# Kernel tuning notes

Measured on AMD Instinct MI355X. Metric: run time of the kernel, lower is better.

Reference implementation:

```python
import jax, jax.numpy as jnp
import numpy as np


def setup_inputs() -> dict:
    key = jax.random.key(0)
    ks = jax.random.split(key, 6)
    B, L, R, A, D = 256, 196, 1024, 512, 2048
    return {
        "h": jax.random.normal(ks[0], (B, R), dtype=jnp.float32),
        "att_feats1": jax.random.normal(ks[1], (B, L, D), dtype=jnp.float32),
        "att_feats2": jax.random.normal(ks[2], (B, L, A), dtype=jnp.float32),
        "att_masks": jnp.ones((B, L), dtype=jnp.float32),
        "W_h": jax.random.normal(ks[3], (R, A), dtype=jnp.float32) * (1.0 / np.sqrt(R)),
        "b_h": jnp.zeros((A,), dtype=jnp.float32),
        "w_a": jax.random.normal(ks[4], (A,), dtype=jnp.float32) * (1.0 / np.sqrt(A)),
        "b_a": jnp.zeros((), dtype=jnp.float32),
    }


def reference(h, att_feats1, att_feats2, att_masks, W_h, b_h, w_a, b_a):
    # att_h = h2att(h): [B, A]
    att_h = h @ W_h + b_h
    # dot = alpha_net(tanh(att_feats2 + att_h[:, None, :])): [B, L]
    dot = jnp.einsum("bla,a->bl", jnp.tanh(att_feats2 + att_h[:, None, :]), w_a) + b_a
    weight = jax.nn.softmax(dot, axis=1)  # [B, L]
    # masked renormalization
    weight = weight * att_masks
    weight = weight / jnp.sum(weight, axis=1, keepdims=True)
    # weighted sum over regions: [B, D]
    att = jnp.einsum("bl,bld->bd", weight, att_feats1)
    return att
```

## Files before the change

kernel.cpp:

```cpp
#include <hip/hip_runtime.h>

#define BB 256
#define LL 196
#define RR 1024
#define AA 512
#define DD 2048

__device__ __forceinline__ float fast_tanh(float x) {
    float e = __expf(2.0f * x);
    return 1.0f - 2.0f * __builtin_amdgcn_rcpf(e + 1.0f);
}

__global__ __launch_bounds__(256) void gemm_hWh(const float* __restrict__ h,
                                                const float* __restrict__ W,
                                                const float* __restrict__ bh,
                                                float* __restrict__ out) {
    __shared__ float As[32][33];
    __shared__ float Bs[32][33];
    const int bn = blockIdx.x;
    const int bm = blockIdx.y;
    const int t  = threadIdx.x;
    const int ty = t >> 4, tx = t & 15;
    const int lr = t >> 3;
    const int lc = (t & 7) * 4;

    float acc00 = 0.f, acc01 = 0.f, acc10 = 0.f, acc11 = 0.f;

    for (int k0 = 0; k0 < RR; k0 += 32) {
        float4 a4 = *(const float4*)&h[(size_t)(bm * 32 + lr) * RR + k0 + lc];
        float4 b4 = *(const float4*)&W[(size_t)(k0 + lr) * AA + bn * 32 + lc];
        As[lr][lc + 0] = a4.x; As[lr][lc + 1] = a4.y;
        As[lr][lc + 2] = a4.z; As[lr][lc + 3] = a4.w;
        Bs[lr][lc + 0] = b4.x; Bs[lr][lc + 1] = b4.y;
        Bs[lr][lc + 2] = b4.z; Bs[lr][lc + 3] = b4.w;
        __syncthreads();
#pragma unroll
        for (int kk = 0; kk < 32; ++kk) {
            float a0 = As[ty * 2 + 0][kk];
            float a1 = As[ty * 2 + 1][kk];
            float b0 = Bs[kk][tx * 2 + 0];
            float b1 = Bs[kk][tx * 2 + 1];
            acc00 += a0 * b0; acc01 += a0 * b1;
            acc10 += a1 * b0; acc11 += a1 * b1;
        }
        __syncthreads();
    }
    const int gm = bm * 32 + ty * 2;
    const int gn = bn * 32 + tx * 2;
    out[(size_t)(gm + 0) * AA + gn + 0] = acc00 + bh[gn + 0];
    out[(size_t)(gm + 0) * AA + gn + 1] = acc01 + bh[gn + 1];
    out[(size_t)(gm + 1) * AA + gn + 0] = acc10 + bh[gn + 0];
    out[(size_t)(gm + 1) * AA + gn + 1] = acc11 + bh[gn + 1];
}

__global__ __launch_bounds__(1024) void attn_fused(
    const float* __restrict__ f1,
    const float* __restrict__ f2,
    const float* __restrict__ masks,
    const float* __restrict__ att_h,
    const float* __restrict__ w_a,
    float* __restrict__ out)
{
    __shared__ float dot[LL];
    __shared__ float red[256];
    __shared__ float w[LL];
    __shared__ float sacc[512 * 4];

    const int b = blockIdx.x;
    const int t = threadIdx.x;
    const int wave = t >> 6, lane = t & 63;

    const float4* ah4 = (const float4*)(att_h + (size_t)b * AA);
    const float4* wa4 = (const float4*)w_a;
    const float4 a0 = ah4[lane * 2], a1 = ah4[lane * 2 + 1];
    const float4 w0 = wa4[lane * 2], w1 = wa4[lane * 2 + 1];

    const float4* f2b = (const float4*)(f2 + (size_t)b * LL * AA);

    for (int l = wave; l < LL; l += 16) {
        float4 v0 = f2b[l * 128 + lane * 2];
        float4 v1 = f2b[l * 128 + lane * 2 + 1];
        float p = fast_tanh(v0.x + a0.x) * w0.x
                + fast_tanh(v0.y + a0.y) * w0.y
                + fast_tanh(v0.z + a0.z) * w0.z
                + fast_tanh(v0.w + a0.w) * w0.w
                + fast_tanh(v1.x + a1.x) * w1.x
                + fast_tanh(v1.y + a1.y) * w1.y
                + fast_tanh(v1.z + a1.z) * w1.z
                + fast_tanh(v1.w + a1.w) * w1.w;
#pragma unroll
        for (int off = 32; off; off >>= 1) p += __shfl_down(p, off);
        if (lane == 0) dot[l] = p;
    }
    __syncthreads();

    if (t < 256) red[t] = (t < LL) ? dot[t] : -1e30f;
    __syncthreads();
#pragma unroll
    for (int s = 128; s; s >>= 1) {
        if (t < s) red[t] = fmaxf(red[t], red[t + s]);
        __syncthreads();
    }
    const float m = red[0];
    __syncthreads();
    float e = 0.f;
    if (t < LL) e = __expf(dot[t] - m) * masks[(size_t)b * LL + t];
    if (t < 256) red[t] = e;
    __syncthreads();
#pragma unroll
    for (int s = 128; s; s >>= 1) {
        if (t < s) red[t] += red[t + s];
        __syncthreads();
    }
    if (t < LL) w[t] = e * (1.0f / red[0]);
    __syncthreads();

    const int u    = t & 511;
    const int half = t >> 9;
    const float4* f1b = (const float4*)(f1 + (size_t)b * LL * DD) + u;
    float4 acc = {0.f, 0.f, 0.f, 0.f};
    const int l0 = half * 98;
#pragma unroll 7
    for (int i = 0; i < 98; ++i) {
        const int l = l0 + i;
        float4 v = f1b[(size_t)l * 512];
        const float wl = w[l];
        acc.x += wl * v.x; acc.y += wl * v.y;
        acc.z += wl * v.z; acc.w += wl * v.w;
    }
    if (half == 1) *(float4*)&sacc[u * 4] = acc;
    __syncthreads();
    if (half == 0) {
        float4 o = *(float4*)&sacc[u * 4];
        acc.x += o.x; acc.y += o.y; acc.z += o.z; acc.w += o.w;
        *(float4*)&out[(size_t)b * DD + u * 4] = acc;
    }
}

extern "C" void kernel_launch(void* const* d_in, const int* in_sizes, int n_in,
                              void* d_out, int out_size, void* d_ws, size_t ws_size,
                              hipStream_t stream) {
    const float* h   = (const float*)d_in[0];
    const float* f1  = (const float*)d_in[1];
    const float* f2  = (const float*)d_in[2];
    const float* msk = (const float*)d_in[3];
    const float* W   = (const float*)d_in[4];
    const float* bh  = (const float*)d_in[5];
    const float* wa  = (const float*)d_in[6];
    float* out = (float*)d_out;

    float* att_h = (float*)d_ws;

    gemm_hWh<<<dim3(16, 8), 256, 0, stream>>>(h, W, bh, att_h);
    attn_fused<<<BB, 1024, 0, stream>>>(f1, f2, msk, att_h, wa, out);
}
```

Before: 634.3 us.

## Fuse h@W_h projection into attention kernel, drop separate GEMM launch

Removes the separate tiled GEMM kernel and computes each batch row's att_h inside the attention block. Each block stages its h row in shared memory and performs a 1024x512 matvec against W_h, split across two thread halves, before the tanh/score phase. This removes a kernel launch and the att_h round trip through global memory. In exchange every block rereads all of W_h (2 MB, likely served from L2) and does the matvec serially ahead of the main streaming work.

```diff
diff --git a/kernel.cpp b/kernel.cpp
--- a/kernel.cpp
+++ b/kernel.cpp
@@ -11,56 +11,18 @@
     return 1.0f - 2.0f * __builtin_amdgcn_rcpf(e + 1.0f);
 }
 
-__global__ __launch_bounds__(256) void gemm_hWh(const float* __restrict__ h,
-                                                const float* __restrict__ W,
-                                                const float* __restrict__ bh,
-                                                float* __restrict__ out) {
-    __shared__ float As[32][33];
-    __shared__ float Bs[32][33];
-    const int bn = blockIdx.x;
-    const int bm = blockIdx.y;
-    const int t  = threadIdx.x;
-    const int ty = t >> 4, tx = t & 15;
-    const int lr = t >> 3;
-    const int lc = (t & 7) * 4;
-
-    float acc00 = 0.f, acc01 = 0.f, acc10 = 0.f, acc11 = 0.f;
-
-    for (int k0 = 0; k0 < RR; k0 += 32) {
-        float4 a4 = *(const float4*)&h[(size_t)(bm * 32 + lr) * RR + k0 + lc];
-        float4 b4 = *(const float4*)&W[(size_t)(k0 + lr) * AA + bn * 32 + lc];
-        As[lr][lc + 0] = a4.x; As[lr][lc + 1] = a4.y;
-        As[lr][lc + 2] = a4.z; As[lr][lc + 3] = a4.w;
-        Bs[lr][lc + 0] = b4.x; Bs[lr][lc + 1] = b4.y;
-        Bs[lr][lc + 2] = b4.z; Bs[lr][lc + 3] = b4.w;
-        __syncthreads();
-#pragma unroll
-        for (int kk = 0; kk < 32; ++kk) {
-            float a0 = As[ty * 2 + 0][kk];
-            float a1 = As[ty * 2 + 1][kk];
-            float b0 = Bs[kk][tx * 2 + 0];
-            float b1 = Bs[kk][tx * 2 + 1];
-            acc00 += a0 * b0; acc01 += a0 * b1;
-            acc10 += a1 * b0; acc11 += a1 * b1;
-        }
-        __syncthreads();
-    }
-    const int gm = bm * 32 + ty * 2;
-    const int gn = bn * 32 + tx * 2;
-    out[(size_t)(gm + 0) * AA + gn + 0] = acc00 + bh[gn + 0];
-    out[(size_t)(gm + 0) * AA + gn + 1] = acc01 + bh[gn + 1];
-    out[(size_t)(gm + 1) * AA + gn + 0] = acc10 + bh[gn + 0];
-    out[(size_t)(gm + 1) * AA + gn + 1] = acc11 + bh[gn + 1];
-}
-
 __global__ __launch_bounds__(1024) void attn_fused(
+    const float* __restrict__ h,
     const float* __restrict__ f1,
     const float* __restrict__ f2,
     const float* __restrict__ masks,
-    const float* __restrict__ att_h,
+    const float* __restrict__ W,
+    const float* __restrict__ bh,
     const float* __restrict__ w_a,
     float* __restrict__ out)
 {
+    __shared__ float hs[RR];
+    __shared__ float ah[AA];
     __shared__ float dot[LL];
     __shared__ float red[256];
     __shared__ float w[LL];
@@ -70,7 +32,30 @@
     const int t = threadIdx.x;
     const int wave = t >> 6, lane = t & 63;
 
-    const float4* ah4 = (const float4*)(att_h + (size_t)b * AA);
+    if (t < 256) ((float4*)hs)[t] = ((const float4*)(h + (size_t)b * RR))[t];
+    __syncthreads();
+
+    {
+        const int n  = t & 511;
+        const int kh = t >> 9;
+        const float4* hs4 = (const float4*)hs;
+        float acc = 0.f;
+#pragma unroll 2
+        for (int k4 = kh * 128; k4 < kh * 128 + 128; ++k4) {
+            const float4 hv = hs4[k4];
+            const float* Wk = W + (size_t)(k4 * 4) * AA + n;
+            acc += hv.x * Wk[0 * AA];
+            acc += hv.y * Wk[1 * AA];
+            acc += hv.z * Wk[2 * AA];
+            acc += hv.w * Wk[3 * AA];
+        }
+        if (kh == 1) sacc[n] = acc;
+        __syncthreads();
+        if (kh == 0) ah[n] = acc + sacc[n] + bh[n];
+    }
+    __syncthreads();
+
+    const float4* ah4 = (const float4*)ah;
     const float4* wa4 = (const float4*)w_a;
     const float4 a0 = ah4[lane * 2], a1 = ah4[lane * 2 + 1];
     const float4 w0 = wa4[lane * 2], w1 = wa4[lane * 2 + 1];
@@ -149,8 +134,5 @@
     const float* wa  = (const float*)d_in[6];
     float* out = (float*)d_out;
 
-    float* att_h = (float*)d_ws;
-
-    gemm_hWh<<<dim3(16, 8), 256, 0, stream>>>(h, W, bh, att_h);
-    attn_fused<<<BB, 1024, 0, stream>>>(f1, f2, msk, att_h, wa, out);
+    attn_fused<<<BB, 1024, 0, stream>>>(h, f1, f2, msk, W, bh, wa, out);
 }
```

Result: no change. 631.3 us (-0.5%).

## Replace two-phase softmax with tiled online softmax overlapping score and feature streams

Applied to the files above, without the earlier changes.

The attention kernel now processes regions in tiles of 16 with an online (running max/sum) softmax. Each tile's scores are computed while the previous tile's weighted f1 accumulation runs, using double-buffered shared memory. This removes the separate max/sum tree reductions and the serialized score-then-gather phases, so f2 and f1 loads can overlap. In exchange it adds per-tile rescaling, a barrier per tile, and exp recomputation by every thread.

```diff
diff --git a/kernel.cpp b/kernel.cpp
--- a/kernel.cpp
+++ b/kernel.cpp
@@ -5,6 +5,7 @@
 #define RR 1024
 #define AA 512
 #define DD 2048
+#define NT 16
 
 __device__ __forceinline__ float fast_tanh(float x) {
     float e = __expf(2.0f * x);
@@ -53,7 +54,7 @@
     out[(size_t)(gm + 1) * AA + gn + 1] = acc11 + bh[gn + 1];
 }
 
-__global__ __launch_bounds__(1024) void attn_fused(
+__global__ __launch_bounds__(1024) void attn_online(
     const float* __restrict__ f1,
     const float* __restrict__ f2,
     const float* __restrict__ masks,
@@ -61,14 +62,14 @@
     const float* __restrict__ w_a,
     float* __restrict__ out)
 {
-    __shared__ float dot[LL];
-    __shared__ float red[256];
-    __shared__ float w[LL];
-    __shared__ float sacc[512 * 4];
+    __shared__ float dots[2][NT];
+    __shared__ float mk[LL];
 
     const int b = blockIdx.x;
     const int t = threadIdx.x;
     const int wave = t >> 6, lane = t & 63;
+
+    if (t < LL) mk[t] = masks[(size_t)b * LL + t];
 
     const float4* ah4 = (const float4*)(att_h + (size_t)b * AA);
     const float4* wa4 = (const float4*)w_a;
@@ -76,65 +77,80 @@
     const float4 w0 = wa4[lane * 2], w1 = wa4[lane * 2 + 1];
 
     const float4* f2b = (const float4*)(f2 + (size_t)b * LL * AA);
+    const float2* f1r = (const float2*)(f1 + (size_t)b * LL * DD) + t;
 
-    for (int l = wave; l < LL; l += 16) {
-        float4 v0 = f2b[l * 128 + lane * 2];
-        float4 v1 = f2b[l * 128 + lane * 2 + 1];
-        float p = fast_tanh(v0.x + a0.x) * w0.x
-                + fast_tanh(v0.y + a0.y) * w0.y
-                + fast_tanh(v0.z + a0.z) * w0.z
-                + fast_tanh(v0.w + a0.w) * w0.w
-                + fast_tanh(v1.x + a1.x) * w1.x
-                + fast_tanh(v1.y + a1.y) * w1.y
-                + fast_tanh(v1.z + a1.z) * w1.z
-                + fast_tanh(v1.w + a1.w) * w1.w;
+    float m = -1e30f, Z = 0.f, accx = 0.f, accy = 0.f;
+
+    auto compute_dots = [&](int ti, float* dbuf) {
+        const int l = ti * NT + wave;
+        float p = -1e30f;
+        if (l < LL) {
+            float4 v0 = f2b[l * 128 + lane * 2];
+            float4 v1 = f2b[l * 128 + lane * 2 + 1];
+            p = fast_tanh(v0.x + a0.x) * w0.x
+              + fast_tanh(v0.y + a0.y) * w0.y
+              + fast_tanh(v0.z + a0.z) * w0.z
+              + fast_tanh(v0.w + a0.w) * w0.w
+              + fast_tanh(v1.x + a1.x) * w1.x
+              + fast_tanh(v1.y + a1.y) * w1.y
+              + fast_tanh(v1.z + a1.z) * w1.z
+              + fast_tanh(v1.w + a1.w) * w1.w;
 #pragma unroll
-        for (int off = 32; off; off >>= 1) p += __shfl_down(p, off);
-        if (lane == 0) dot[l] = p;
-    }
+            for (int off = 32; off; off >>= 1) p += __shfl_down(p, off);
+        }
+        if (lane == 0) dbuf[wave] = p;
+    };
+
+    compute_dots(0, dots[0]);
     __syncthreads();
 
-    if (t < 256) red[t] = (t < LL) ? dot[t] : -1e30f;
-    __syncthreads();
+    for (int ti = 0; ti < 12; ++ti) {
+        compute_dots(ti + 1, dots[(ti + 1) & 1]);
+
+        const float* db = dots[ti & 1];
+        const int l0 = ti * NT;
+        float d[NT], tmax = -1e30f;
 #pragma unroll
-    for (int s = 128; s; s >>= 1) {
-        if (t < s) red[t] = fmaxf(red[t], red[t + s]);
+        for (int j = 0; j < NT; ++j) { d[j] = db[j]; tmax = fmaxf(tmax, d[j]); }
+        const float mn = fmaxf(m, tmax);
+        const float alpha = __expf(m - mn);
+        float e[NT], zt = 0.f;
+#pragma unroll
+        for (int j = 0; j < NT; ++j) { e[j] = __expf(d[j] - mn) * mk[l0 + j]; zt += e[j]; }
+        Z = Z * alpha + zt;
+        accx *= alpha; accy *= alpha;
+#pragma unroll
+        for (int j = 0; j < NT; ++j) {
+            float2 v = f1r[(size_t)(l0 + j) * (DD / 2)];
+            accx += e[j] * v.x; accy += e[j] * v.y;
+        }
+        m = mn;
         __syncthreads();
     }
-    const float m = red[0];
-    __syncthreads();
-    float e = 0.f;
-    if (t < LL) e = __expf(dot[t] - m) * masks[(size_t)b * LL + t];
-    if (t < 256) red[t] = e;
-    __syncthreads();
+
+    {
+        const float* db = dots[0];
+        const int l0 = 192;
+        float d[4], tmax = -1e30f;
 #pragma unroll
-    for (int s = 128; s; s >>= 1) {
-        if (t < s) red[t] += red[t + s];
-        __syncthreads();
+        for (int j = 0; j < 4; ++j) { d[j] = db[j]; tmax = fmaxf(tmax, d[j]); }
+        const float mn = fmaxf(m, tmax);
+        const float alpha = __expf(m - mn);
+        float e[4], zt = 0.f;
+#pragma unroll
+        for (int j = 0; j < 4; ++j) { e[j] = __expf(d[j] - mn) * mk[l0 + j]; zt += e[j]; }
+        Z = Z * alpha + zt;
+        accx *= alpha; accy *= alpha;
+#pragma unroll
+        for (int j = 0; j < 4; ++j) {
+            float2 v = f1r[(size_t)(l0 + j) * (DD / 2)];
+            accx += e[j] * v.x; accy += e[j] * v.y;
+        }
     }
-    if (t < LL) w[t] = e * (1.0f / red[0]);
-    __syncthreads();
 
-    const int u    = t & 511;
-    const int half = t >> 9;
-    const float4* f1b = (const float4*)(f1 + (size_t)b * LL * DD) + u;
-    float4 acc = {0.f, 0.f, 0.f, 0.f};
-    const int l0 = half * 98;
-#pragma unroll 7
-    for (int i = 0; i < 98; ++i) {
-        const int l = l0 + i;
-        float4 v = f1b[(size_t)l * 512];
-        const float wl = w[l];
-        acc.x += wl * v.x; acc.y += wl * v.y;
-        acc.z += wl * v.z; acc.w += wl * v.w;
-    }
-    if (half == 1) *(float4*)&sacc[u * 4] = acc;
-    __syncthreads();
-    if (half == 0) {
-        float4 o = *(float4*)&sacc[u * 4];
-        acc.x += o.x; acc.y += o.y; acc.z += o.z; acc.w += o.w;
-        *(float4*)&out[(size_t)b * DD + u * 4] = acc;
-    }
+    const float invZ = 1.0f / Z;
+    float2 o; o.x = accx * invZ; o.y = accy * invZ;
+    ((float2*)(out + (size_t)b * DD))[t] = o;
 }
 
 extern "C" void kernel_launch(void* const* d_in, const int* in_sizes, int n_in,
@@ -152,5 +168,5 @@
     float* att_h = (float*)d_ws;
 
     gemm_hWh<<<dim3(16, 8), 256, 0, stream>>>(h, W, bh, att_h);
-    attn_fused<<<BB, 1024, 0, stream>>>(f1, f2, msk, att_h, wa, out);
+    attn_online<<<BB, 1024, 0, stream>>>(f1, f2, msk, att_h, wa, out);
 }
```

Result: no change. 634.0 us (-0.0%).
